# Kernel tuning notes

Measured on AMD Instinct MI355X. Metric: run time of the kernel, lower is better.

## Reference

```python
import jax, jax.numpy as jnp
import numpy as np

NH = 32          # nh * 2 neighbors per point (init nh=16)
P_REDUCTION = 0.5


def setup_inputs() -> dict:
    key = jax.random.key(0)
    k1, k2 = jax.random.split(key)
    x = jax.random.normal(k1, (2, 8192, 256), dtype=jnp.float32)       # [b, n, e]
    coords = jax.random.normal(k2, (2, 2, 8192, 1), dtype=jnp.float32) # [b, c, n, 1]
    return {"x": x, "coords": coords}


def _knn_gather(x, coords):
    """Return features of the NH nearest neighbors of each point: [b, n, NH, e]."""
    cs = coords[..., 0]                                   # [b, c, n]
    sq = jnp.sum(cs * cs, axis=1)                         # [b, n]
    # squared euclidean distances [b, n, n]
    d2 = sq[:, :, None] + sq[:, None, :] - 2.0 * jnp.einsum('bcn,bcm->bnm', cs, cs)
    d2 = jax.lax.stop_gradient(d2)                        # indices are non-differentiable
    _, nn_idx = jax.lax.top_k(-d2, NH)                    # [b, n, NH] nearest points
    # gather neighbor features: [b, 1, n, e] indexed with [b, n, NH, 1] -> [b, n, NH, e]
    x_nh = jnp.take_along_axis(x[:, None, :, :], nn_idx[..., None], axis=2)
    return x_nh


def _forward(x, coords):
    b, n, e = x.shape
    x_nh = _knn_gather(x, coords)                         # [b, n, NH, e]
    # unbiased std over the neighbor dim (torch.std default, ddof=1)
    mean_nh = jnp.mean(x_nh, axis=-2, keepdims=True)
    local_s = jnp.sqrt(jnp.sum((x_nh - mean_nh) ** 2, axis=-2) / (NH - 1))  # [b, n, e]
    global_m = jnp.abs(jnp.mean(x, axis=1))               # [b, e]
    local_dist = jnp.sum(local_s / global_m[:, None, :], axis=-1)           # [b, n]
    n_keep = int((1.0 - P_REDUCTION) * n)
    _, keep_idx = jax.lax.top_k(local_dist, n_keep)       # [b, n_keep], sorted desc
    x_out = jnp.take_along_axis(x, keep_idx[:, :, None], axis=1)            # [b, n_keep, e]
    coords_out = jnp.take_along_axis(coords, keep_idx[:, None, :, None], axis=2)  # [b, c, n_keep, 1]
    return x_out, coords_out, local_dist


def reference(x, coords):
    return _forward(x, coords)
```

## Files before the change

### kernel.cpp

```cpp
#include <hip/hip_runtime.h>

#define NN 8192
#define EE 256
#define KNH 32
#define NKEEP 4096
#define NCX 64
#define NCELL 4096
#define CNT_MIN 48

typedef unsigned long long u64;
typedef unsigned int u32;


__device__ __forceinline__ int cellof(float v) {
    const int q = (int)floorf((v + 4.6f) * (64.0f / 9.2f));
    return min(max(q, 0), NCX - 1);
}

__global__ void __launch_bounds__(1024) k_pre(const float* __restrict__ coords,
                                              const float* __restrict__ x,
                                              int* __restrict__ start,
                                              float2* __restrict__ sc,
                                              int* __restrict__ sj,
                                              float* __restrict__ part) {
    __shared__ int cnt[NCELL];
    __shared__ int wsum[16];
    const int blk = blockIdx.x;
    if (blk >= 2) {
        float* fred = (float*)cnt;
        const int unit  = blk - 2;
        const int b     = unit >> 5;
        const int chunk = unit & 31;
        const int col   = threadIdx.x & 255;
        const int qtr   = threadIdx.x >> 8;
        const float* xp = x + ((size_t)b * NN + (size_t)chunk * 256 + (size_t)qtr * 64) * EE + col;
        float s = 0.0f;
        for (int r = 0; r < 64; ++r) s += xp[(size_t)r * EE];
        fred[threadIdx.x] = s;
        __syncthreads();
        if (threadIdx.x < 256) {
            const float tot = fred[threadIdx.x] + fred[threadIdx.x + 256]
                            + fred[threadIdx.x + 512] + fred[threadIdx.x + 768];
            part[((size_t)b * 32 + chunk) * EE + threadIdx.x] = tot;
        }
        return;
    }
    const int b = blk, t = threadIdx.x;
    const int lane = t & 63, wv = t >> 6;
#pragma unroll
    for (int k = 0; k < 4; ++k) cnt[k * 1024 + t] = 0;
    __syncthreads();
#pragma unroll
    for (int k = 0; k < 8; ++k) {
        const int i = k * 1024 + t;
        const float xv = coords[(size_t)b * 2 * NN + i];
        const float yv = coords[(size_t)b * 2 * NN + NN + i];
        atomicAdd(&cnt[cellof(xv) * NCX + cellof(yv)], 1);
    }
    __syncthreads();
    const int v0 = cnt[t * 4 + 0], v1 = cnt[t * 4 + 1];
    const int v2 = cnt[t * 4 + 2], v3 = cnt[t * 4 + 3];
    const int s = v0 + v1 + v2 + v3;
    int inc = s;
#pragma unroll
    for (int d = 1; d < 64; d <<= 1) {
        const int u = __shfl_up(inc, d);
        inc += (lane >= d) ? u : 0;
    }
    if (lane == 63) wsum[wv] = inc;
    __syncthreads();
    int wpre = 0;
#pragma unroll
    for (int w = 0; w < 16; ++w) wpre += (w < wv) ? wsum[w] : 0;
    int run = wpre + inc - s;
    start[b * (NCELL + 1) + t * 4 + 0] = run; cnt[t * 4 + 0] = run; run += v0;
    start[b * (NCELL + 1) + t * 4 + 1] = run; cnt[t * 4 + 1] = run; run += v1;
    start[b * (NCELL + 1) + t * 4 + 2] = run; cnt[t * 4 + 2] = run; run += v2;
    start[b * (NCELL + 1) + t * 4 + 3] = run; cnt[t * 4 + 3] = run; run += v3;
    if (t == 0) start[b * (NCELL + 1) + NCELL] = NN;
    __syncthreads();
#pragma unroll
    for (int k = 0; k < 8; ++k) {
        const int i = k * 1024 + t;
        const float xv = coords[(size_t)b * 2 * NN + i];
        const float yv = coords[(size_t)b * 2 * NN + NN + i];
        const int p = atomicAdd(&cnt[cellof(xv) * NCX + cellof(yv)], 1);
        sc[(size_t)b * NN + p] = make_float2(xv, yv);
        sj[(size_t)b * NN + p] = i;
    }
}

__global__ void k_gm_final(const float* __restrict__ part, float* __restrict__ gm) {
    const int b = blockIdx.y, t = threadIdx.x;
    float s = 0.0f;
    for (int c = 0; c < 32; ++c) s += part[((size_t)b * 32 + c) * EE + t];
    gm[b * EE + t] = fabsf(s / (float)NN);
}

__device__ __forceinline__ u64 shfl_xor_u64(u64 v, int m) {
    const u32 hi = (u32)__shfl_xor((int)(u32)(v >> 32), m);
    const u32 lo = (u32)__shfl_xor((int)(u32)v, m);
    return ((u64)hi << 32) | lo;
}

__device__ __forceinline__ u64 wave_min_u64(u64 h) {
#pragma unroll
    for (int s = 1; s < 64; s <<= 1) {
        const u64 o = shfl_xor_u64(h, s);
        h = (o < h) ? o : h;
    }
    return h;
}

__device__ __noinline__ int exact_fb(const float2* scb, const int* sjb, const int* stb,
                                     float cx, float cy, int xl, int xh, int yl, int yh,
                                     int lane) {
    const int nsl = xh - xl + 1;
    int c0 = 0, c1 = 0;
    if (lane < nsl) { c0 = stb[(xl + lane) * NCX + yl]; c1 = stb[(xl + lane) * NCX + yh + 1]; }
    const int myc = c0, len = c1 - c0;
    int inc = len;
#pragma unroll
    for (int d = 1; d < 64; d <<= 1) {
        const int v = __shfl_up(inc, d);
        inc += (lane >= d) ? v : 0;
    }
    const int ex = inc - len;
    const int L = __shfl(inc, 63);
    int jk = 0;
    u64 minkeep = 0;
    for (int k = 0; k < KNH; ++k) {
        u64 best = ~0ull;
        for (int g = 0; g < L; g += 64) {
            const int gp = g + lane;
            int lo = 0, hi = nsl - 1;
#pragma unroll
            for (int st = 0; st < 6; ++st) {
                const int mid = (lo + hi + 1) >> 1;
                const int v = __shfl(ex, mid);
                const bool go = (v <= gp);
                lo = go ? mid : lo;
                hi = go ? hi : mid - 1;
            }
            const int cnd = __shfl(myc, lo) + gp - __shfl(ex, lo);
            const int cc = min(max(cnd, 0), NN - 1);
            const float2 pt = scb[cc];
            const int jj = sjb[cc];
            const float dx = cx - pt.x, dy = cy - pt.y;
            const float d = fmaf(dx, dx, dy * dy);
            const u64 kk = ((u64)__float_as_uint(d) << 32) | (u32)jj;
            if (gp < L && kk >= minkeep && kk < best) best = kk;
        }
        const u64 h = wave_min_u64(best);
        if (lane == k) jk = (int)(u32)h;
        minkeep = h + 1;
    }
    return jk;
}

__global__ void __launch_bounds__(256) k_knn_dist(
        const float* __restrict__ x,
        const float* __restrict__ gm, const float2* __restrict__ sc,
        const int* __restrict__ sj, const int* __restrict__ start,
        float* __restrict__ ld_out) {
    __shared__ u64 comp[4][64];
    const int wg   = blockIdx.x;
    const int swz  = (wg & 7) * 512 + (wg >> 3);
    const int b    = swz >> 11;
    const int pb   = swz & 2047;
    const int wid  = threadIdx.x >> 6;
    const int lane = threadIdx.x & 63;
    const int p    = pb * 4 + wid;

    const float2* scb = sc + (size_t)b * NN;
    const int*    sjb = sj + (size_t)b * NN;
    const int*    stb = start + b * (NCELL + 1);
    const float2 cp = scb[p];
    const int    i  = sjb[p];
    const float ci0 = cp.x, ci1 = cp.y;
    const int qx = cellof(ci0), qy = cellof(ci1);

    int xl, yl, yh, nsl;
    int myc0 = 0, mylen = 0;
    {
        const int xl0 = max(qx - 1, 0), xh0 = min(qx + 1, NCX - 1);
        const int yl0 = max(qy - 1, 0), yh0 = min(qy + 1, NCX - 1);
        const int ns0 = xh0 - xl0 + 1;
        int a0 = 0, a1 = 0;
        if (lane < ns0) { a0 = stb[(xl0 + lane) * NCX + yl0]; a1 = stb[(xl0 + lane) * NCX + yh0 + 1]; }
        const int xl1 = max(qx - 2, 0), xh1 = min(qx + 2, NCX - 1);
        const int yl1 = max(qy - 2, 0), yh1 = min(qy + 2, NCX - 1);
        const int ns1 = xh1 - xl1 + 1;
        int b0 = 0, b1 = 0;
        if (lane < ns1) { b0 = stb[(xl1 + lane) * NCX + yl1]; b1 = stb[(xl1 + lane) * NCX + yh1 + 1]; }
        const int xl2 = max(qx - 4, 0), xh2c = min(qx + 4, NCX - 1);
        const int yl2 = max(qy - 4, 0), yh2c = min(qy + 4, NCX - 1);
        const int ns2 = xh2c - xl2 + 1;
        int e0 = 0, e1 = 0;
        if (lane < ns2) { e0 = stb[(xl2 + lane) * NCX + yl2]; e1 = stb[(xl2 + lane) * NCX + yh2c + 1]; }

        const int l0 = a1 - a0, l1 = b1 - b0, l2 = e1 - e0;
        int t0 = l0, t1 = l1, t2 = l2;
#pragma unroll
        for (int s = 1; s < 64; s <<= 1) {
            t0 += __shfl_xor(t0, s);
            t1 += __shfl_xor(t1, s);
            t2 += __shfl_xor(t2, s);
        }
        if (t0 >= CNT_MIN) {
            xl = xl0; yl = yl0; yh = yh0; nsl = ns0; myc0 = a0; mylen = l0;
        } else if (t1 >= CNT_MIN) {
            xl = xl1; yl = yl1; yh = yh1; nsl = ns1; myc0 = b0; mylen = l1;
        } else if (t2 >= CNT_MIN) {
            xl = xl2; yl = yl2; yh = yh2c; nsl = ns2; myc0 = e0; mylen = l2;
        } else {
            int r = 8;
            for (;;) {
                xl = max(qx - r, 0);
                const int xh = min(qx + r, NCX - 1);
                yl = max(qy - r, 0);
                yh = min(qy + r, NCX - 1);
                nsl = xh - xl + 1;
                int c0 = 0, c1 = 0;
                if (lane < nsl) {
                    c0 = stb[(xl + lane) * NCX + yl];
                    c1 = stb[(xl + lane) * NCX + yh + 1];
                }
                myc0 = c0; mylen = c1 - c0;
                int tot = mylen;
#pragma unroll
                for (int s = 1; s < 64; s <<= 1) tot += __shfl_xor(tot, s);
                if (tot >= CNT_MIN || r >= NCX) break;
                r <<= 1;
            }
        }
    }
    const int xh1box = xl + nsl - 1;
    int incl = mylen;
#pragma unroll
    for (int d = 1; d < 64; d <<= 1) {
        const int v = __shfl_up(incl, d);
        incl += (lane >= d) ? v : 0;
    }
    int excl = incl - mylen;
    const int L1 = __shfl(incl, 63);

    float dmin = 1e30f;
    u32 kdb0 = 0xFFFFFFFFu, kdb1 = 0xFFFFFFFFu, kdb2 = 0xFFFFFFFFu, kdb3 = 0xFFFFFFFFu;
    int  kjj0 = 0, kjj1 = 0, kjj2 = 0, kjj3 = 0;

#define CHUNK2(G, DB0, JJ0, DB1, JJ1)                                       \
    do {                                                                    \
        const int gp0 = (G) + lane;                                         \
        const int gp1 = (G) + 64 + lane;                                    \
        int lo0 = 0, hi0 = nsl - 1, lo1 = 0, hi1 = nsl - 1;                 \
        _Pragma("unroll")                                                   \
        for (int st = 0; st < 6; ++st) {                                    \
            const int mid0 = (lo0 + hi0 + 1) >> 1;                          \
            const int mid1 = (lo1 + hi1 + 1) >> 1;                          \
            const int v0 = __shfl(excl, mid0);                              \
            const int v1 = __shfl(excl, mid1);                              \
            const bool go0 = (v0 <= gp0), go1 = (v1 <= gp1);                \
            lo0 = go0 ? mid0 : lo0; hi0 = go0 ? hi0 : mid0 - 1;             \
            lo1 = go1 ? mid1 : lo1; hi1 = go1 ? hi1 : mid1 - 1;             \
        }                                                                   \
        const int cnd0 = __shfl(myc0, lo0) + gp0 - __shfl(excl, lo0);       \
        const int cnd1 = __shfl(myc0, lo1) + gp1 - __shfl(excl, lo1);       \
        const int cc0 = min(max(cnd0, 0), NN - 1);                          \
        const int cc1 = min(max(cnd1, 0), NN - 1);                          \
        const float2 pt0 = scb[cc0];                                        \
        const float2 pt1 = scb[cc1];                                        \
        const int j0_ = sjb[cc0];                                           \
        const int j1_ = sjb[cc1];                                           \
        const float dx0 = ci0 - pt0.x, dy0 = ci1 - pt0.y;                   \
        const float dx1 = ci0 - pt1.x, dy1 = ci1 - pt1.y;                   \
        const float d0 = fmaf(dx0, dx0, dy0 * dy0);                         \
        const float d1 = fmaf(dx1, dx1, dy1 * dy1);                         \
        if (gp0 < L1) { dmin = fminf(dmin, d0); DB0 = __float_as_uint(d0); JJ0 = j0_; } \
        if (gp1 < L1) { dmin = fminf(dmin, d1); DB1 = __float_as_uint(d1); JJ1 = j1_; } \
    } while (0)

    CHUNK2(0, kdb0, kjj0, kdb1, kjj1);
    if (L1 > 128) CHUNK2(128, kdb2, kjj2, kdb3, kjj3);
    for (int g = 256; g < L1; g += 128) {
        const int gp0 = g + lane;
        const int gp1 = g + 64 + lane;
        int lo0 = 0, hi0 = nsl - 1, lo1 = 0, hi1 = nsl - 1;
#pragma unroll
        for (int st = 0; st < 6; ++st) {
            const int mid0 = (lo0 + hi0 + 1) >> 1;
            const int mid1 = (lo1 + hi1 + 1) >> 1;
            const int v0 = __shfl(excl, mid0);
            const int v1 = __shfl(excl, mid1);
            const bool go0 = (v0 <= gp0), go1 = (v1 <= gp1);
            lo0 = go0 ? mid0 : lo0; hi0 = go0 ? hi0 : mid0 - 1;
            lo1 = go1 ? mid1 : lo1; hi1 = go1 ? hi1 : mid1 - 1;
        }
        const int cnd0 = __shfl(myc0, lo0) + gp0 - __shfl(excl, lo0);
        const int cnd1 = __shfl(myc0, lo1) + gp1 - __shfl(excl, lo1);
        const int cc0 = min(max(cnd0, 0), NN - 1);
        const int cc1 = min(max(cnd1, 0), NN - 1);
        const float2 pt0 = scb[cc0];
        const float2 pt1 = scb[cc1];
        const float dx0 = ci0 - pt0.x, dy0 = ci1 - pt0.y;
        const float dx1 = ci0 - pt1.x, dy1 = ci1 - pt1.y;
        const float d0 = fmaf(dx0, dx0, dy0 * dy0);
        const float d1 = fmaf(dx1, dx1, dy1 * dy1);
        if (gp0 < L1) dmin = fminf(dmin, d0);
        if (gp1 < L1) dmin = fminf(dmin, d1);
    }

    u32 mk = __float_as_uint(dmin);
#pragma unroll
    for (int k = 2; k <= 64; k <<= 1) {
#pragma unroll
        for (int j = k >> 1; j > 0; j >>= 1) {
            const u32 o = (u32)__shfl_xor((int)mk, j);
            const bool keep_min = (((lane & j) == 0) == ((lane & k) == 0));
            const u32 mn = min(mk, o), mx = max(mk, o);
            mk = keep_min ? mn : mx;
        }
    }
    const u32 T = (u32)__shfl((int)mk, 31);

    const float srad = sqrtf(__uint_as_float(T)) * 1.0002f + 1e-5f;
    const int p2xl = cellof(ci0 - srad), p2xh = cellof(ci0 + srad);
    const int p2yl = cellof(ci1 - srad), p2yh = cellof(ci1 + srad);
    const bool contained = (L1 <= 256) && (p2xl >= xl) && (p2xh <= xh1box) &&
                           (p2yl >= yl) && (p2yh <= yh);

    const u64 lmask = (1ull << lane) - 1;
    int base = 0;

#define COMPACT(DB, JJ)                                                     \
    do {                                                                    \
        const bool keep = ((DB) <= T);                                      \
        const u64 m = __ballot(keep);                                       \
        const int pos = base + __popcll(m & lmask);                         \
        base += __popcll(m);                                                \
        if (keep && pos < 64) comp[wid][pos] = ((u64)(DB) << 32) | (u32)(JJ); \
    } while (0)

    if (contained) {
        COMPACT(kdb0, kjj0);
        COMPACT(kdb1, kjj1);
        COMPACT(kdb2, kjj2);
        COMPACT(kdb3, kjj3);
    } else {
        const int nsl2 = p2xh - p2xl + 1;
        int c0 = 0, c1 = 0;
        if (lane < nsl2) {
            c0 = stb[(p2xl + lane) * NCX + p2yl];
            c1 = stb[(p2xl + lane) * NCX + p2yh + 1];
        }
        const int myc2 = c0;
        const int len2 = c1 - c0;
        int incl2 = len2;
#pragma unroll
        for (int d = 1; d < 64; d <<= 1) {
            const int v = __shfl_up(incl2, d);
            incl2 += (lane >= d) ? v : 0;
        }
        const int excl2 = incl2 - len2;
        const int L2 = __shfl(incl2, 63);
        for (int g = 0; g < L2; g += 64) {
            const int gp = g + lane;
            int lo = 0, hi = nsl2 - 1;
#pragma unroll
            for (int st = 0; st < 6; ++st) {
                const int mid = (lo + hi + 1) >> 1;
                const int v = __shfl(excl2, mid);
                const bool go = (v <= gp);
                lo = go ? mid : lo;
                hi = go ? hi : mid - 1;
            }
            const int cnd = __shfl(myc2, lo) + gp - __shfl(excl2, lo);
            const int cc  = min(max(cnd, 0), NN - 1);
            const float2 pt = scb[cc];
            const int    jj = sjb[cc];
            const float dx = ci0 - pt.x, dy = ci1 - pt.y;
            const u32 db = __float_as_uint(fmaf(dx, dx, dy * dy));
            const bool keep = (gp < L2) && (db <= T);
            const u64 m = __ballot(keep);
            const int pos = base + __popcll(m & lmask);
            base += __popcll(m);
            if (keep && pos < 64) comp[wid][pos] = ((u64)db << 32) | (u32)jj;
        }
    }
    const bool ovf = (base > 64) || (base < KNH);

    u64 key = (lane < base) ? comp[wid][lane] : ~0ull;
#pragma unroll
    for (int k = 2; k <= 64; k <<= 1) {
#pragma unroll
        for (int j = k >> 1; j > 0; j >>= 1) {
            const u64 other = shfl_xor_u64(key, j);
            const bool keep_min = (((lane & j) == 0) == ((lane & k) == 0));
            const bool lt = (key < other);
            const u64 mn = lt ? key : other;
            const u64 mx = lt ? other : key;
            key = keep_min ? mn : mx;
        }
    }
    int jkeep = (int)(u32)key;

    if (ovf) jkeep = exact_fb(scb, sjb, stb, ci0, ci1, p2xl, p2xh, p2yl, p2yh, lane);

    float s1[4] = {0.f, 0.f, 0.f, 0.f};
    float s2[4] = {0.f, 0.f, 0.f, 0.f};
    const float* xb = x + (size_t)b * NN * EE;
#pragma unroll 8
    for (int k = 0; k < KNH; ++k) {
        const int j = __builtin_amdgcn_readlane(jkeep, k);
        const float4 v = *reinterpret_cast<const float4*>(xb + (size_t)j * EE + (lane << 2));
        s1[0] += v.x; s2[0] += v.x * v.x;
        s1[1] += v.y; s2[1] += v.y * v.y;
        s1[2] += v.z; s2[2] += v.z * v.z;
        s1[3] += v.w; s2[3] += v.w * v.w;
    }

    const float* gmb = gm + b * EE;
    float tt = 0.f;
#pragma unroll
    for (int q = 0; q < 4; ++q) {
        const float sum = s1[q];
        float ssd = s2[q] - sum * sum * (1.0f / 32.0f);
        ssd = ssd > 0.f ? ssd : 0.f;
        const float ls = sqrtf(ssd * (1.0f / 31.0f));
        tt += ls / gmb[(lane << 2) + q];
    }
#pragma unroll
    for (int s2r = 1; s2r < 64; s2r <<= 1) tt += __shfl_xor(tt, s2r);

    if (lane == 0) ld_out[(size_t)b * NN + i] = tt;
}

__global__ void k_rank_gather(const float* __restrict__ x, const float* __restrict__ coords,
                              const float* __restrict__ ld,
                              float* __restrict__ x_out, float* __restrict__ c_out) {
    const int b    = blockIdx.y;
    const int wid  = threadIdx.x >> 6;
    const int lane = threadIdx.x & 63;
    const int i    = blockIdx.x * 4 + wid;
    const float* lb = ld + (size_t)b * NN;
    const float di = lb[i];
    int cnt = 0;
    for (int t = 0; t < NN / 256; ++t) {
        const int j0 = t * 256 + (lane << 2);
        const float4 dv = *reinterpret_cast<const float4*>(lb + j0);
        cnt += (dv.x > di || (dv.x == di && (j0 + 0) < i)) ? 1 : 0;
        cnt += (dv.y > di || (dv.y == di && (j0 + 1) < i)) ? 1 : 0;
        cnt += (dv.z > di || (dv.z == di && (j0 + 2) < i)) ? 1 : 0;
        cnt += (dv.w > di || (dv.w == di && (j0 + 3) < i)) ? 1 : 0;
    }
#pragma unroll
    for (int s = 1; s < 64; s <<= 1) cnt += __shfl_xor(cnt, s);

    if (cnt < NKEEP) {
        const float4 v = *reinterpret_cast<const float4*>(x + ((size_t)b * NN + i) * EE + (lane << 2));
        *reinterpret_cast<float4*>(x_out + ((size_t)b * NKEEP + cnt) * EE + (lane << 2)) = v;
        if (lane < 2) {
            c_out[((size_t)b * 2 + lane) * NKEEP + cnt] = coords[((size_t)b * 2 + lane) * NN + i];
        }
    }
}

extern "C" void kernel_launch(void* const* d_in, const int* in_sizes, int n_in,
                              void* d_out, int out_size, void* d_ws, size_t ws_size,
                              hipStream_t stream) {
    const float* x      = (const float*)d_in[0];
    const float* coords = (const float*)d_in[1];

    float* out    = (float*)d_out;
    float* x_out  = out;
    float* c_out  = out + 2097152;
    float* ld_out = out + 2113536;

    char*   ws    = (char*)d_ws;
    float*  part  = (float*)(ws);
    float*  gm    = (float*)(ws + 65536);
    int*    start = (int*)  (ws + 67584);
    float2* sc    = (float2*)(ws + 100384);
    int*    sj    = (int*)  (ws + 231456);

    k_pre        <<<66,            1024, 0, stream>>>(coords, x, start, sc, sj, part);
    k_gm_final   <<<dim3(1, 2),    256,  0, stream>>>(part, gm);
    k_knn_dist   <<<4096,          256,  0, stream>>>(x, gm, sc, sj, start, ld_out);
    k_rank_gather<<<dim3(2048, 2), 256,  0, stream>>>(x, coords, ld_out, x_out, c_out);
}
```

Measured before the change: 82.90 us.

## Replace prefix-sum binary search candidate mapping with per-strip cell iteration

Removes the wave prefix scan and the per-lane 6-step shuffle binary search that mapped a flat candidate index to a grid strip. Candidates are now visited strip by strip: each strip's start and length are broadcast, and lanes walk contiguous points. The first pass rotates lane assignment so partial chunks fill the wave's four cached register slots, and containment is gated on whether everything fit in four chunks. This cuts shuffle and ALU work per candidate, but can leave lanes idle on short strips and adds more loop iterations when strips are numerous and small.

```diff
diff --git a/kernel.cpp b/kernel.cpp
--- a/kernel.cpp
+++ b/kernel.cpp
@@ -116,40 +116,28 @@
                                      float cx, float cy, int xl, int xh, int yl, int yh,
                                      int lane) {
     const int nsl = xh - xl + 1;
-    int c0 = 0, c1 = 0;
-    if (lane < nsl) { c0 = stb[(xl + lane) * NCX + yl]; c1 = stb[(xl + lane) * NCX + yh + 1]; }
-    const int myc = c0, len = c1 - c0;
-    int inc = len;
-#pragma unroll
-    for (int d = 1; d < 64; d <<= 1) {
-        const int v = __shfl_up(inc, d);
-        inc += (lane >= d) ? v : 0;
-    }
-    const int ex = inc - len;
-    const int L = __shfl(inc, 63);
+    int c0 = 0, len = 0;
+    if (lane < nsl) {
+        const int a = stb[(xl + lane) * NCX + yl];
+        const int e = stb[(xl + lane) * NCX + yh + 1];
+        c0 = a; len = e - a;
+    }
     int jk = 0;
     u64 minkeep = 0;
     for (int k = 0; k < KNH; ++k) {
         u64 best = ~0ull;
-        for (int g = 0; g < L; g += 64) {
-            const int gp = g + lane;
-            int lo = 0, hi = nsl - 1;
-#pragma unroll
-            for (int st = 0; st < 6; ++st) {
-                const int mid = (lo + hi + 1) >> 1;
-                const int v = __shfl(ex, mid);
-                const bool go = (v <= gp);
-                lo = go ? mid : lo;
-                hi = go ? hi : mid - 1;
+        for (int s = 0; s < nsl; ++s) {
+            const int sc0 = __shfl(c0, s);
+            const int sl  = __shfl(len, s);
+            for (int u = lane; u < sl; u += 64) {
+                const int cc = min(sc0 + u, NN - 1);
+                const float2 pt = scb[cc];
+                const int jj = sjb[cc];
+                const float dx = cx - pt.x, dy = cy - pt.y;
+                const float d = fmaf(dx, dx, dy * dy);
+                const u64 kk = ((u64)__float_as_uint(d) << 32) | (u32)jj;
+                if (kk >= minkeep && kk < best) best = kk;
             }
-            const int cnd = __shfl(myc, lo) + gp - __shfl(ex, lo);
-            const int cc = min(max(cnd, 0), NN - 1);
-            const float2 pt = scb[cc];
-            const int jj = sjb[cc];
-            const float dx = cx - pt.x, dy = cy - pt.y;
-            const float d = fmaf(dx, dx, dy * dy);
-            const u64 kk = ((u64)__float_as_uint(d) << 32) | (u32)jj;
-            if (gp < L && kk >= minkeep && kk < best) best = kk;
         }
         const u64 h = wave_min_u64(best);
         if (lane == k) jk = (int)(u32)h;
@@ -236,79 +224,36 @@
         }
     }
     const int xh1box = xl + nsl - 1;
-    int incl = mylen;
-#pragma unroll
-    for (int d = 1; d < 64; d <<= 1) {
-        const int v = __shfl_up(incl, d);
-        incl += (lane >= d) ? v : 0;
-    }
-    int excl = incl - mylen;
-    const int L1 = __shfl(incl, 63);
 
     float dmin = 1e30f;
     u32 kdb0 = 0xFFFFFFFFu, kdb1 = 0xFFFFFFFFu, kdb2 = 0xFFFFFFFFu, kdb3 = 0xFFFFFFFFu;
     int  kjj0 = 0, kjj1 = 0, kjj2 = 0, kjj3 = 0;
-
-#define CHUNK2(G, DB0, JJ0, DB1, JJ1)                                       \
-    do {                                                                    \
-        const int gp0 = (G) + lane;                                         \
-        const int gp1 = (G) + 64 + lane;                                    \
-        int lo0 = 0, hi0 = nsl - 1, lo1 = 0, hi1 = nsl - 1;                 \
-        _Pragma("unroll")                                                   \
-        for (int st = 0; st < 6; ++st) {                                    \
-            const int mid0 = (lo0 + hi0 + 1) >> 1;                          \
-            const int mid1 = (lo1 + hi1 + 1) >> 1;                          \
-            const int v0 = __shfl(excl, mid0);                              \
-            const int v1 = __shfl(excl, mid1);                              \
-            const bool go0 = (v0 <= gp0), go1 = (v1 <= gp1);                \
-            lo0 = go0 ? mid0 : lo0; hi0 = go0 ? hi0 : mid0 - 1;             \
-            lo1 = go1 ? mid1 : lo1; hi1 = go1 ? hi1 : mid1 - 1;             \
-        }                                                                   \
-        const int cnd0 = __shfl(myc0, lo0) + gp0 - __shfl(excl, lo0);       \
-        const int cnd1 = __shfl(myc0, lo1) + gp1 - __shfl(excl, lo1);       \
-        const int cc0 = min(max(cnd0, 0), NN - 1);                          \
-        const int cc1 = min(max(cnd1, 0), NN - 1);                          \
-        const float2 pt0 = scb[cc0];                                        \
-        const float2 pt1 = scb[cc1];                                        \
-        const int j0_ = sjb[cc0];                                           \
-        const int j1_ = sjb[cc1];                                           \
-        const float dx0 = ci0 - pt0.x, dy0 = ci1 - pt0.y;                   \
-        const float dx1 = ci0 - pt1.x, dy1 = ci1 - pt1.y;                   \
-        const float d0 = fmaf(dx0, dx0, dy0 * dy0);                         \
-        const float d1 = fmaf(dx1, dx1, dy1 * dy1);                         \
-        if (gp0 < L1) { dmin = fminf(dmin, d0); DB0 = __float_as_uint(d0); JJ0 = j0_; } \
-        if (gp1 < L1) { dmin = fminf(dmin, d1); DB1 = __float_as_uint(d1); JJ1 = j1_; } \
-    } while (0)
-
-    CHUNK2(0, kdb0, kjj0, kdb1, kjj1);
-    if (L1 > 128) CHUNK2(128, kdb2, kjj2, kdb3, kjj3);
-    for (int g = 256; g < L1; g += 128) {
-        const int gp0 = g + lane;
-        const int gp1 = g + 64 + lane;
-        int lo0 = 0, hi0 = nsl - 1, lo1 = 0, hi1 = nsl - 1;
-#pragma unroll
-        for (int st = 0; st < 6; ++st) {
-            const int mid0 = (lo0 + hi0 + 1) >> 1;
-            const int mid1 = (lo1 + hi1 + 1) >> 1;
-            const int v0 = __shfl(excl, mid0);
-            const int v1 = __shfl(excl, mid1);
-            const bool go0 = (v0 <= gp0), go1 = (v1 <= gp1);
-            lo0 = go0 ? mid0 : lo0; hi0 = go0 ? hi0 : mid0 - 1;
-            lo1 = go1 ? mid1 : lo1; hi1 = go1 ? hi1 : mid1 - 1;
-        }
-        const int cnd0 = __shfl(myc0, lo0) + gp0 - __shfl(excl, lo0);
-        const int cnd1 = __shfl(myc0, lo1) + gp1 - __shfl(excl, lo1);
-        const int cc0 = min(max(cnd0, 0), NN - 1);
-        const int cc1 = min(max(cnd1, 0), NN - 1);
-        const float2 pt0 = scb[cc0];
-        const float2 pt1 = scb[cc1];
-        const float dx0 = ci0 - pt0.x, dy0 = ci1 - pt0.y;
-        const float dx1 = ci0 - pt1.x, dy1 = ci1 - pt1.y;
-        const float d0 = fmaf(dx0, dx0, dy0 * dy0);
-        const float d1 = fmaf(dx1, dx1, dy1 * dy1);
-        if (gp0 < L1) dmin = fminf(dmin, d0);
-        if (gp1 < L1) dmin = fminf(dmin, d1);
-    }
+    int rot = 0, ccount = 0;
+    for (int s = 0; s < nsl; ++s) {
+        const int sc0 = __shfl(myc0, s);
+        const int sl  = __shfl(mylen, s);
+        for (int done = 0; done < sl; done += 64) {
+            const int clen = min(sl - done, 64);
+            const int q = (lane - rot) & 63;
+            const bool act = q < clen;
+            const int cc = min(sc0 + done + q, NN - 1);
+            const float2 pt = scb[cc];
+            const float dx = ci0 - pt.x, dy = ci1 - pt.y;
+            const float d = fmaf(dx, dx, dy * dy);
+            const u32 db = act ? __float_as_uint(d) : 0xFFFFFFFFu;
+            if (act) dmin = fminf(dmin, d);
+            if (ccount < 4) {
+                const int jj = sjb[cc];
+                if (ccount == 0)      { kdb0 = db; kjj0 = jj; }
+                else if (ccount == 1) { kdb1 = db; kjj1 = jj; }
+                else if (ccount == 2) { kdb2 = db; kjj2 = jj; }
+                else                  { kdb3 = db; kjj3 = jj; }
+            }
+            ++ccount;
+            rot = (rot + clen) & 63;
+        }
+    }
+    const bool cacheok = (ccount <= 4);
 
     u32 mk = __float_as_uint(dmin);
 #pragma unroll
@@ -326,7 +271,7 @@
     const float srad = sqrtf(__uint_as_float(T)) * 1.0002f + 1e-5f;
     const int p2xl = cellof(ci0 - srad), p2xh = cellof(ci0 + srad);
     const int p2yl = cellof(ci1 - srad), p2yh = cellof(ci1 + srad);
-    const bool contained = (L1 <= 256) && (p2xl >= xl) && (p2xh <= xh1box) &&
+    const bool contained = cacheok && (p2xl >= xl) && (p2xh <= xh1box) &&
                            (p2yl >= yl) && (p2yh <= yh);
 
     const u64 lmask = (1ull << lane) - 1;
@@ -348,43 +293,29 @@
         COMPACT(kdb3, kjj3);
     } else {
         const int nsl2 = p2xh - p2xl + 1;
-        int c0 = 0, c1 = 0;
+        int c02 = 0, len2 = 0;
         if (lane < nsl2) {
-            c0 = stb[(p2xl + lane) * NCX + p2yl];
-            c1 = stb[(p2xl + lane) * NCX + p2yh + 1];
-        }
-        const int myc2 = c0;
-        const int len2 = c1 - c0;
-        int incl2 = len2;
-#pragma unroll
-        for (int d = 1; d < 64; d <<= 1) {
-            const int v = __shfl_up(incl2, d);
-            incl2 += (lane >= d) ? v : 0;
-        }
-        const int excl2 = incl2 - len2;
-        const int L2 = __shfl(incl2, 63);
-        for (int g = 0; g < L2; g += 64) {
-            const int gp = g + lane;
-            int lo = 0, hi = nsl2 - 1;
-#pragma unroll
-            for (int st = 0; st < 6; ++st) {
-                const int mid = (lo + hi + 1) >> 1;
-                const int v = __shfl(excl2, mid);
-                const bool go = (v <= gp);
-                lo = go ? mid : lo;
-                hi = go ? hi : mid - 1;
+            const int a = stb[(p2xl + lane) * NCX + p2yl];
+            const int e = stb[(p2xl + lane) * NCX + p2yh + 1];
+            c02 = a; len2 = e - a;
+        }
+        for (int s = 0; s < nsl2; ++s) {
+            const int sc0 = __shfl(c02, s);
+            const int sl  = __shfl(len2, s);
+            for (int done = 0; done < sl; done += 64) {
+                const int clen = min(sl - done, 64);
+                const bool act = lane < clen;
+                const int cc = min(sc0 + done + lane, NN - 1);
+                const float2 pt = scb[cc];
+                const int jj = sjb[cc];
+                const float dx = ci0 - pt.x, dy = ci1 - pt.y;
+                const u32 db = __float_as_uint(fmaf(dx, dx, dy * dy));
+                const bool keep = act && (db <= T);
+                const u64 m = __ballot(keep);
+                const int pos = base + __popcll(m & lmask);
+                base += __popcll(m);
+                if (keep && pos < 64) comp[wid][pos] = ((u64)db << 32) | (u32)jj;
             }
-            const int cnd = __shfl(myc2, lo) + gp - __shfl(excl2, lo);
-            const int cc  = min(max(cnd, 0), NN - 1);
-            const float2 pt = scb[cc];
-            const int    jj = sjb[cc];
-            const float dx = ci0 - pt.x, dy = ci1 - pt.y;
-            const u32 db = __float_as_uint(fmaf(dx, dx, dy * dy));
-            const bool keep = (gp < L2) && (db <= T);
-            const u64 m = __ballot(keep);
-            const int pos = base + __popcll(m & lmask);
-            base += __popcll(m);
-            if (keep && pos < 64) comp[wid][pos] = ((u64)db << 32) | (u32)jj;
         }
     }
     const bool ovf = (base > 64) || (base < KNH);
```

Result: slower. 91.93 us (+10.9%).
